# Optimization experiments

Measured on AMD Instinct MI355X. Metric: run time of the kernel, lower is better.

The kernel has to match this reference:

```python
import jax, jax.numpy as jnp
import numpy as np

NUM_GRAPHS = 1000


def setup_inputs() -> dict:
    key = jax.random.key(0)
    ks = jax.random.split(key, 8)
    N, E, F_IN, H = 100000, 1600000, 128, 64
    x = jax.random.normal(ks[0], (N, F_IN), dtype=jnp.float32)
    edge_index = jax.random.randint(ks[1], (2, E), 0, N, dtype=jnp.int64)
    batch = jnp.sort(jax.random.randint(ks[2], (N,), 0, NUM_GRAPHS, dtype=jnp.int64))
    # Glorot-ish scaled weights
    W1 = jax.random.normal(ks[3], (F_IN, H), dtype=jnp.float32) / np.sqrt(F_IN)
    W2 = jax.random.normal(ks[4], (H, H), dtype=jnp.float32) / np.sqrt(H)
    W3 = jax.random.normal(ks[5], (H, H), dtype=jnp.float32) / np.sqrt(H)
    Wl = jax.random.normal(ks[6], (H, 1), dtype=jnp.float32) / np.sqrt(H)
    return {
        "x": x, "edge_index": edge_index, "batch": batch,
        "W1": W1, "b1": jnp.zeros((H,), jnp.float32),
        "W2": W2, "b2": jnp.zeros((H,), jnp.float32),
        "W3": W3, "b3": jnp.zeros((H,), jnp.float32),
        "Wl": Wl, "bl": jnp.zeros((1,), jnp.float32),
    }


def _gcn_prep(edge_index, n_nodes):
    """Add self-loops and compute symmetric normalization coefficients."""
    loops = jnp.arange(n_nodes, dtype=edge_index.dtype)
    src = jnp.concatenate([edge_index[0], loops])  # [E+N]
    dst = jnp.concatenate([edge_index[1], loops])  # [E+N]
    deg = jax.ops.segment_sum(jnp.ones_like(dst, dtype=jnp.float32), dst,
                              num_segments=n_nodes)
    dinv = jnp.where(deg > 0, jax.lax.rsqrt(jnp.maximum(deg, 1.0)), 0.0)
    norm = dinv[src] * dinv[dst]  # [E+N]
    return src, dst, norm


def _gcn_conv(h, W, b, src, dst, norm, n_nodes):
    h = h @ W                              # [N, H] linear transform first
    msg = h[src] * norm[:, None]           # gather + normalize
    agg = jax.ops.segment_sum(msg, dst, num_segments=n_nodes)  # scatter-add
    return agg + b


def reference(x, edge_index, batch, W1, b1, W2, b2, W3, b3, Wl, bl):
    n_nodes = x.shape[0]
    src, dst, norm = _gcn_prep(edge_index, n_nodes)
    h = jax.nn.relu(_gcn_conv(x, W1, b1, src, dst, norm, n_nodes))
    h = jax.nn.relu(_gcn_conv(h, W2, b2, src, dst, norm, n_nodes))
    h = _gcn_conv(h, W3, b3, src, dst, norm, n_nodes)
    # global_mean_pool over graphs
    sums = jax.ops.segment_sum(h, batch, num_segments=NUM_GRAPHS)
    cnts = jax.ops.segment_sum(jnp.ones((n_nodes,), jnp.float32), batch,
                               num_segments=NUM_GRAPHS)
    pooled = sums / jnp.maximum(cnts, 1.0)[:, None]
    # dropout is identity in eval mode
    return pooled @ Wl + bl
```

## Files before the change

### kernel.cpp

```cpp
#include <hip/hip_runtime.h>
#include <stdint.h>

#define BKT 1024
#define EPB 8192

typedef __attribute__((ext_vector_type(8))) __bf16 bf16x8;
typedef __attribute__((ext_vector_type(4))) float floatx4;

__device__ __forceinline__ float bf2f(unsigned short h) {
    return __uint_as_float(((unsigned)h) << 16);
}
__device__ __forceinline__ float4 bf4(ushort4 v) {
    return make_float4(bf2f(v.x), bf2f(v.y), bf2f(v.z), bf2f(v.w));
}
__device__ __forceinline__ unsigned short f2bf(float f) {
    unsigned u = __float_as_uint(f);
    u = u + 0x7FFFu + ((u >> 16) & 1u);
    return (unsigned short)(u >> 16);
}
__device__ __forceinline__ ushort4 pack4(float a, float b, float c, float d) {
    ushort4 r; r.x = f2bf(a); r.y = f2bf(b); r.z = f2bf(c); r.w = f2bf(d); return r;
}


__global__ void w3l_kernel(const float* __restrict__ W3, const float* __restrict__ Wl,
                           float* __restrict__ w3l) {
    int k = threadIdx.x;
    float s = 0.f;
#pragma unroll 16
    for (int c = 0; c < 64; ++c) s += W3[k * 64 + c] * Wl[c];
    w3l[k] = s;
}


__global__ __launch_bounds__(256) void coarse_hist(const int* __restrict__ dst,
                                                   int* __restrict__ coarse, int E, int NBK) {
    __shared__ int h[128];
    if (threadIdx.x < 128) h[threadIdx.x] = 0;
    __syncthreads();
    int stride = gridDim.x * 256;
    int gid = blockIdx.x * 256 + threadIdx.x;
    const int4* d4 = (const int4*)dst;
    int E4 = E >> 2;
    for (int i = gid; i < E4; i += stride) {
        int4 v = d4[i];
        atomicAdd(&h[v.x >> 10], 1);
        atomicAdd(&h[v.y >> 10], 1);
        atomicAdd(&h[v.z >> 10], 1);
        atomicAdd(&h[v.w >> 10], 1);
    }
    for (int i = (E4 << 2) + gid; i < E; i += stride)
        atomicAdd(&h[dst[i] >> 10], 1);
    __syncthreads();
    if (threadIdx.x < NBK) {
        int v = h[threadIdx.x];
        if (v) atomicAdd(&coarse[threadIdx.x], v);
    }
}

__global__ void coarse_scan(const int* __restrict__ coarse, int* __restrict__ bbase,
                            int NBK, int E) {
    if (threadIdx.x == 0 && blockIdx.x == 0) {
        int run = 0;
        for (int i = 0; i < NBK; ++i) { bbase[i] = run; run += coarse[i]; }
        bbase[NBK] = E;
    }
}


__global__ __launch_bounds__(256) void partition_kernel(const int* __restrict__ src,
                                                        const int* __restrict__ dst,
                                                        const int* __restrict__ bbase,
                                                        int* __restrict__ gbcur,
                                                        unsigned* __restrict__ pairs,
                                                        int E, int NBK) {
    __shared__ unsigned stage[EPB];
    __shared__ int hist[128], offs[129], gbase[128], lcur[128];
    int base = blockIdx.x * EPB;
    int cntE = min(EPB, E - base);
    if (threadIdx.x < 128) hist[threadIdx.x] = 0;
    __syncthreads();
    {
        const int4* d4 = (const int4*)(dst + base);
        int c4 = cntE >> 2;
        for (int i = threadIdx.x; i < c4; i += 256) {
            int4 v = d4[i];
            atomicAdd(&hist[v.x >> 10], 1);
            atomicAdd(&hist[v.y >> 10], 1);
            atomicAdd(&hist[v.z >> 10], 1);
            atomicAdd(&hist[v.w >> 10], 1);
        }
        for (int i = (c4 << 2) + (int)threadIdx.x; i < cntE; i += 256)
            atomicAdd(&hist[dst[base + i] >> 10], 1);
    }
    __syncthreads();
    if (threadIdx.x == 0) {
        int run = 0;
        for (int b = 0; b < NBK; ++b) { offs[b] = run; run += hist[b]; }
        offs[NBK] = run;
    }
    __syncthreads();
    if (threadIdx.x < NBK) {
        int b = threadIdx.x;
        int h = hist[b];
        if (h > 0) gbase[b] = bbase[b] + atomicAdd(&gbcur[b << 4], h);
        lcur[b] = offs[b];
    }
    __syncthreads();
    for (int i = threadIdx.x; i < cntE; i += 256) {
        int e = base + i;
        int d = dst[e];
        int b = d >> 10;
        int slot = atomicAdd(&lcur[b], 1);
        stage[slot] = ((unsigned)src[e] << 10) | (unsigned)(d & 1023);
    }
    __syncthreads();
    int total = offs[NBK];
    for (int j = threadIdx.x; j < total; j += 256) {
        int lo = 0, hi = NBK;
        while (lo < hi) { int mid = (lo + hi) >> 1; if (offs[mid + 1] <= j) lo = mid + 1; else hi = mid; }
        pairs[gbase[lo] + (j - offs[lo])] = stage[j];
    }
}


__global__ __launch_bounds__(256) void bucket_build(const unsigned* __restrict__ pairs,
                                                    const int* __restrict__ bbase,
                                                    int* __restrict__ rowptr,
                                                    int* __restrict__ csr, int N, int E) {
    __shared__ int cnt[BKT];
    __shared__ int psum[256];
    int b = blockIdx.x;
    int nbase = b << 10;
    int pbeg = bbase[b], pend = bbase[b + 1];
    for (int i = threadIdx.x; i < BKT; i += 256) cnt[i] = 0;
    __syncthreads();
    for (int j = pbeg + (int)threadIdx.x; j < pend; j += 256)
        atomicAdd(&cnt[pairs[j] & 1023u], 1);
    __syncthreads();
    int i0 = threadIdx.x * 4;
    int c0 = cnt[i0], c1 = cnt[i0 + 1], c2 = cnt[i0 + 2], c3 = cnt[i0 + 3];
    int local = c0 + c1 + c2 + c3;
    psum[threadIdx.x] = local;
    __syncthreads();
    for (int d = 1; d < 256; d <<= 1) {
        int t = (threadIdx.x >= d) ? psum[threadIdx.x - d] : 0;
        __syncthreads();
        psum[threadIdx.x] += t;
        __syncthreads();
    }
    int excl = psum[threadIdx.x] - local;
    int o0 = pbeg + excl;
    int o1 = o0 + c0, o2 = o1 + c1, o3 = o2 + c2;
    int n0 = nbase + i0;
    if (n0 < N)     rowptr[n0]     = o0;
    if (n0 + 1 < N) rowptr[n0 + 1] = o1;
    if (n0 + 2 < N) rowptr[n0 + 2] = o2;
    if (n0 + 3 < N) rowptr[n0 + 3] = o3;
    cnt[i0] = o0; cnt[i0 + 1] = o1; cnt[i0 + 2] = o2; cnt[i0 + 3] = o3;
    __syncthreads();
    for (int j = pbeg + (int)threadIdx.x; j < pend; j += 256) {
        unsigned p = pairs[j];
        int slot = atomicAdd(&cnt[p & 1023u], 1);
        csr[slot] = (int)(p >> 10);
    }
    if (b == 0 && threadIdx.x == 0) rowptr[N] = E;
}


__global__ __launch_bounds__(256) void gemm1_mfma(const float* __restrict__ X,
                                                  const float* __restrict__ W,
                                                  const int* __restrict__ rowptr,
                                                  __bf16* __restrict__ gbh, int N) {
    __shared__ __align__(16) __bf16 Wt[64][136];
    for (int i = threadIdx.x; i < 128 * 64; i += 256) {
        int k = i >> 6, c = i & 63;
        Wt[c][k] = (__bf16)W[i];
    }
    __syncthreads();

    int wave = threadIdx.x >> 6;
    int l = threadIdx.x & 63;
    int cidx = l & 15;
    int g = l >> 4;
    int wbase = blockIdx.x * 64 + wave * 16;

    int arow = wbase + cidx;
    int arowc = min(arow, N - 1);
    const float4* xr = (const float4*)(X + (size_t)arowc * 128);
    bf16x8 afr[4];
#pragma unroll
    for (int kb = 0; kb < 4; ++kb) {
        float4 p = xr[kb * 8 + g * 2];
        float4 q = xr[kb * 8 + g * 2 + 1];
        bf16x8 a;
        a[0] = (__bf16)p.x; a[1] = (__bf16)p.y; a[2] = (__bf16)p.z; a[3] = (__bf16)p.w;
        a[4] = (__bf16)q.x; a[5] = (__bf16)q.y; a[6] = (__bf16)q.z; a[7] = (__bf16)q.w;
        afr[kb] = a;
    }

    floatx4 acc[4];
#pragma unroll
    for (int ct = 0; ct < 4; ++ct) acc[ct] = (floatx4){0.f, 0.f, 0.f, 0.f};

#pragma unroll
    for (int ct = 0; ct < 4; ++ct) {
#pragma unroll
        for (int kb = 0; kb < 4; ++kb) {
            bf16x8 bfr = *(const bf16x8*)&Wt[ct * 16 + cidx][kb * 32 + g * 8];
            acc[ct] = __builtin_amdgcn_mfma_f32_16x16x32_bf16(afr[kb], bfr, acc[ct], 0, 0, 0);
        }
    }

    int r0 = wbase + g * 4;
    int rp[5];
#pragma unroll
    for (int i = 0; i < 5; ++i) rp[i] = rowptr[min(r0 + i, N)];
#pragma unroll
    for (int i = 0; i < 4; ++i) {
        int row = r0 + i;
        if (row < N) {
            float dv = rsqrtf((float)(rp[i + 1] - rp[i]) + 1.0f);
#pragma unroll
            for (int ct = 0; ct < 4; ++ct)
                gbh[(size_t)row * 64 + ct * 16 + cidx] = (__bf16)(acc[ct][i] * dv);
        }
    }
}


__global__ __launch_bounds__(256) void gather_relu_kernel(const ushort4* __restrict__ gb,
                                                          const int* __restrict__ rowptr,
                                                          const int* __restrict__ csr,
                                                          const float* __restrict__ bias,
                                                          ushort4* __restrict__ h, int N) {
    int tid = blockIdx.x * blockDim.x + threadIdx.x;
    int node = tid >> 4;
    if (node >= N) return;
    int t = tid & 15;
    int beg = rowptr[node], end = rowptr[node + 1];
    float dinv = rsqrtf((float)(end - beg) + 1.0f);
    float4 acc = bf4(gb[(size_t)node * 16 + t]);
    int j = beg;
    for (; j + 8 <= end; j += 8) {
        int s0 = csr[j], s1 = csr[j + 1], s2 = csr[j + 2], s3 = csr[j + 3];
        int s4 = csr[j + 4], s5 = csr[j + 5], s6 = csr[j + 6], s7 = csr[j + 7];
        float4 v0 = bf4(gb[(size_t)s0 * 16 + t]);
        float4 v1 = bf4(gb[(size_t)s1 * 16 + t]);
        float4 v2 = bf4(gb[(size_t)s2 * 16 + t]);
        float4 v3 = bf4(gb[(size_t)s3 * 16 + t]);
        float4 v4 = bf4(gb[(size_t)s4 * 16 + t]);
        float4 v5 = bf4(gb[(size_t)s5 * 16 + t]);
        float4 v6 = bf4(gb[(size_t)s6 * 16 + t]);
        float4 v7 = bf4(gb[(size_t)s7 * 16 + t]);
        acc.x += ((v0.x + v1.x) + (v2.x + v3.x)) + ((v4.x + v5.x) + (v6.x + v7.x));
        acc.y += ((v0.y + v1.y) + (v2.y + v3.y)) + ((v4.y + v5.y) + (v6.y + v7.y));
        acc.z += ((v0.z + v1.z) + (v2.z + v3.z)) + ((v4.z + v5.z) + (v6.z + v7.z));
        acc.w += ((v0.w + v1.w) + (v2.w + v3.w)) + ((v4.w + v5.w) + (v6.w + v7.w));
    }
    for (; j + 2 <= end; j += 2) {
        int s0 = csr[j], s1 = csr[j + 1];
        float4 v0 = bf4(gb[(size_t)s0 * 16 + t]);
        float4 v1 = bf4(gb[(size_t)s1 * 16 + t]);
        acc.x += v0.x + v1.x; acc.y += v0.y + v1.y;
        acc.z += v0.z + v1.z; acc.w += v0.w + v1.w;
    }
    if (j < end) {
        int s0 = csr[j];
        float4 v0 = bf4(gb[(size_t)s0 * 16 + t]);
        acc.x += v0.x; acc.y += v0.y; acc.z += v0.z; acc.w += v0.w;
    }
    float4 bb = *(const float4*)&bias[t * 4];
    h[(size_t)node * 16 + t] = pack4(fmaxf(acc.x * dinv + bb.x, 0.f),
                                     fmaxf(acc.y * dinv + bb.y, 0.f),
                                     fmaxf(acc.z * dinv + bb.z, 0.f),
                                     fmaxf(acc.w * dinv + bb.w, 0.f));
}


__global__ __launch_bounds__(256) void gemm64_mfma(const __bf16* __restrict__ H,
                                                   const float* __restrict__ W,
                                                   const int* __restrict__ rowptr,
                                                   __bf16* __restrict__ out, int N) {
    __shared__ __align__(16) __bf16 Wt[64][72];
    for (int i = threadIdx.x; i < 64 * 64; i += 256) {
        int k = i >> 6, c = i & 63;
        Wt[c][k] = (__bf16)W[i];
    }
    __syncthreads();

    int wave = threadIdx.x >> 6;
    int l = threadIdx.x & 63;
    int cidx = l & 15;
    int g = l >> 4;
    int wbase = blockIdx.x * 64 + wave * 16;

    int arow = wbase + cidx;
    int arowc = min(arow, N - 1);
    const bf16x8* hr = (const bf16x8*)(H + (size_t)arowc * 64);
    bf16x8 afr[2];
#pragma unroll
    for (int kb = 0; kb < 2; ++kb) afr[kb] = hr[kb * 4 + g];

    floatx4 acc[4];
#pragma unroll
    for (int ct = 0; ct < 4; ++ct) acc[ct] = (floatx4){0.f, 0.f, 0.f, 0.f};

#pragma unroll
    for (int ct = 0; ct < 4; ++ct) {
#pragma unroll
        for (int kb = 0; kb < 2; ++kb) {
            bf16x8 bfr = *(const bf16x8*)&Wt[ct * 16 + cidx][kb * 32 + g * 8];
            acc[ct] = __builtin_amdgcn_mfma_f32_16x16x32_bf16(afr[kb], bfr, acc[ct], 0, 0, 0);
        }
    }

    int r0 = wbase + g * 4;
    int rp[5];
#pragma unroll
    for (int i = 0; i < 5; ++i) rp[i] = rowptr[min(r0 + i, N)];
#pragma unroll
    for (int i = 0; i < 4; ++i) {
        int row = r0 + i;
        if (row < N) {
            float dv = rsqrtf((float)(rp[i + 1] - rp[i]) + 1.0f);
#pragma unroll
            for (int ct = 0; ct < 4; ++ct)
                out[(size_t)row * 64 + ct * 16 + cidx] = (__bf16)(acc[ct][i] * dv);
        }
    }
}


__global__ __launch_bounds__(256) void agg_dot2_kernel(const ushort4* __restrict__ gb,
                                                       const int* __restrict__ rowptr,
                                                       const int* __restrict__ csr,
                                                       const float* __restrict__ bias,
                                                       const float* __restrict__ w3l,
                                                       float* __restrict__ p, int N) {
    int tid = blockIdx.x * blockDim.x + threadIdx.x;
    int node = tid >> 4;
    if (node >= N) return;
    int t = tid & 15;
    int beg = rowptr[node], end = rowptr[node + 1];
    float dinv = rsqrtf((float)(end - beg) + 1.0f);
    float4 acc = bf4(gb[(size_t)node * 16 + t]);
    int j = beg;
    for (; j + 8 <= end; j += 8) {
        int s0 = csr[j], s1 = csr[j + 1], s2 = csr[j + 2], s3 = csr[j + 3];
        int s4 = csr[j + 4], s5 = csr[j + 5], s6 = csr[j + 6], s7 = csr[j + 7];
        float4 v0 = bf4(gb[(size_t)s0 * 16 + t]);
        float4 v1 = bf4(gb[(size_t)s1 * 16 + t]);
        float4 v2 = bf4(gb[(size_t)s2 * 16 + t]);
        float4 v3 = bf4(gb[(size_t)s3 * 16 + t]);
        float4 v4 = bf4(gb[(size_t)s4 * 16 + t]);
        float4 v5 = bf4(gb[(size_t)s5 * 16 + t]);
        float4 v6 = bf4(gb[(size_t)s6 * 16 + t]);
        float4 v7 = bf4(gb[(size_t)s7 * 16 + t]);
        acc.x += ((v0.x + v1.x) + (v2.x + v3.x)) + ((v4.x + v5.x) + (v6.x + v7.x));
        acc.y += ((v0.y + v1.y) + (v2.y + v3.y)) + ((v4.y + v5.y) + (v6.y + v7.y));
        acc.z += ((v0.z + v1.z) + (v2.z + v3.z)) + ((v4.z + v5.z) + (v6.z + v7.z));
        acc.w += ((v0.w + v1.w) + (v2.w + v3.w)) + ((v4.w + v5.w) + (v6.w + v7.w));
    }
    for (; j + 2 <= end; j += 2) {
        int s0 = csr[j], s1 = csr[j + 1];
        float4 v0 = bf4(gb[(size_t)s0 * 16 + t]);
        float4 v1 = bf4(gb[(size_t)s1 * 16 + t]);
        acc.x += v0.x + v1.x; acc.y += v0.y + v1.y;
        acc.z += v0.z + v1.z; acc.w += v0.w + v1.w;
    }
    if (j < end) {
        int s0 = csr[j];
        float4 v0 = bf4(gb[(size_t)s0 * 16 + t]);
        acc.x += v0.x; acc.y += v0.y; acc.z += v0.z; acc.w += v0.w;
    }
    float4 bb = *(const float4*)&bias[t * 4];
    float4 wv = *(const float4*)&w3l[t * 4];
    float hx = fmaxf(acc.x * dinv + bb.x, 0.f);
    float hy = fmaxf(acc.y * dinv + bb.y, 0.f);
    float hz = fmaxf(acc.z * dinv + bb.z, 0.f);
    float hw = fmaxf(acc.w * dinv + bb.w, 0.f);
    float s = (hx * wv.x + hy * wv.y) + (hz * wv.z + hw * wv.w);
    s += __shfl_xor(s, 1);
    s += __shfl_xor(s, 2);
    s += __shfl_xor(s, 4);
    s += __shfl_xor(s, 8);
    if (t == 0) p[node] = s * dinv;
}


__global__ __launch_bounds__(256) void scalar_agg(const float* __restrict__ p,
                                                  const int* __restrict__ rowptr,
                                                  const int* __restrict__ csr,
                                                  float* __restrict__ s_node, int N) {
    int n = blockIdx.x * 256 + threadIdx.x;
    if (n >= N) return;
    int beg = rowptr[n], end = rowptr[n + 1];
    float dinv = rsqrtf((float)(end - beg) + 1.0f);
    float acc = p[n];
    int j = beg;
    for (; j + 4 <= end; j += 4) {
        float a0 = p[csr[j]], a1 = p[csr[j + 1]], a2 = p[csr[j + 2]], a3 = p[csr[j + 3]];
        acc += (a0 + a1) + (a2 + a3);
    }
    for (; j < end; ++j) acc += p[csr[j]];
    s_node[n] = acc * dinv;
}


__device__ __forceinline__ int lower_bound_dev(const int* __restrict__ a, int n, int v) {
    int lo = 0, hi = n;
    while (lo < hi) { int mid = (lo + hi) >> 1; if (a[mid] < v) lo = mid + 1; else hi = mid; }
    return lo;
}

__global__ void pool_out_kernel(const float* __restrict__ s_node, const int* __restrict__ batch,
                                const float* __restrict__ b3, const float* __restrict__ Wl,
                                const float* __restrict__ bl, float* __restrict__ out, int N) {
    float v = b3[threadIdx.x] * Wl[threadIdx.x];
    for (int d = 32; d; d >>= 1) v += __shfl_down(v, d);
    float bldot = __shfl(v, 0, 64);

    int gidx = blockIdx.x;
    int lo = lower_bound_dev(batch, N, gidx);
    int hi = lower_bound_dev(batch, N, gidx + 1);
    float s = 0.f;
    for (int i = lo + threadIdx.x; i < hi; i += 64) s += s_node[i];
    for (int d = 32; d; d >>= 1) s += __shfl_down(s, d);
    if (threadIdx.x == 0)
        out[gidx] = s / fmaxf((float)(hi - lo), 1.0f) + bldot + bl[0];
}


extern "C" void kernel_launch(void* const* d_in, const int* in_sizes, int n_in,
                              void* d_out, int out_size, void* d_ws, size_t ws_size,
                              hipStream_t stream) {
    const float* x   = (const float*)d_in[0];
    const int*   ei  = (const int*)d_in[1];
    const int*   bat = (const int*)d_in[2];
    const float* W1  = (const float*)d_in[3];
    const float* b1  = (const float*)d_in[4];
    const float* W2  = (const float*)d_in[5];
    const float* b2  = (const float*)d_in[6];
    const float* W3  = (const float*)d_in[7];
    const float* b3  = (const float*)d_in[8];
    const float* Wl  = (const float*)d_in[9];
    const float* bl  = (const float*)d_in[10];

    const int N = in_sizes[0] / 128;
    const int E = in_sizes[1] / 2;
    const int G = out_size;

    const int* src = ei;
    const int* dst = ei + E;

    const int NBK = (N + BKT - 1) / BKT;
    const int Np = (N + 4) & ~3;

    int*      rowptr = (int*)d_ws;
    int*      coarse = rowptr + Np;
    int*      bbase  = coarse + 128;
    float*    w3l    = (float*)(bbase + 132);
    int*      gbcur  = (int*)(w3l + 64);
    int*      csr    = gbcur + (size_t)NBK * 16;
    unsigned* pairs  = (unsigned*)(csr + E);
    ushort4*  gbA    = (ushort4*)(pairs + E);
    ushort4*  gbB    = gbA + (size_t)N * 16;
    ushort4*  hbuf   = gbB + (size_t)N * 16;
    float*    pbuf   = (float*)(hbuf + (size_t)N * 16);
    float*    s_node = pbuf + N;

    hipMemsetAsync(coarse, 0, (324 + (size_t)NBK * 16) * sizeof(int), stream);
    w3l_kernel<<<1, 64, 0, stream>>>(W3, Wl, w3l);
    coarse_hist<<<256, 256, 0, stream>>>(dst, coarse, E, NBK);
    coarse_scan<<<1, 64, 0, stream>>>(coarse, bbase, NBK, E);
    partition_kernel<<<(E + EPB - 1) / EPB, 256, 0, stream>>>(src, dst, bbase, gbcur, pairs, E, NBK);
    bucket_build<<<NBK, 256, 0, stream>>>(pairs, bbase, rowptr, csr, N, E);

    const int aggGrid = (int)(((size_t)N * 16 + 255) / 256);

    gemm1_mfma<<<(N + 63) / 64, 256, 0, stream>>>(x, W1, rowptr, (__bf16*)gbA, N);
    gather_relu_kernel<<<aggGrid, 256, 0, stream>>>(gbA, rowptr, csr, b1, hbuf, N);
    gemm64_mfma<<<(N + 63) / 64, 256, 0, stream>>>((const __bf16*)hbuf, W2, rowptr, (__bf16*)gbB, N);
    agg_dot2_kernel<<<aggGrid, 256, 0, stream>>>(gbB, rowptr, csr, b2, w3l, pbuf, N);
    scalar_agg<<<(N + 255) / 256, 256, 0, stream>>>(pbuf, rowptr, csr, s_node, N);
    pool_out_kernel<<<G, 64, 0, stream>>>(s_node, bat, b3, Wl, bl, (float*)d_out, N);
}
```

Measured before the change: 244.4 us.

## Merge w3l into scan kernel, use nontemporal CSR loads/stores, halve partition tile

Four things change. The tiny w3l kernel is folded into the single-block scan kernel, which removes one launch. CSR index loads in the aggregation kernels become nontemporal loads, and the relu output is written as one packed 64-bit nontemporal store, so streaming traffic does less damage to the cache holding the gathered features. EPB drops from 8192 to 4096, which doubles the partition grid and halves its shared-memory staging. Risks: nontemporal hints may do nothing or may hurt reuse of h by the next GEMM, and smaller partition blocks mean more global atomic contention.

```diff
diff --git a/kernel.cpp b/kernel.cpp
--- a/kernel.cpp
+++ b/kernel.cpp
@@ -2,7 +2,7 @@
 #include <stdint.h>
 
 #define BKT 1024
-#define EPB 8192
+#define EPB 4096
 
 typedef __attribute__((ext_vector_type(8))) __bf16 bf16x8;
 typedef __attribute__((ext_vector_type(4))) float floatx4;
@@ -18,18 +18,8 @@
     u = u + 0x7FFFu + ((u >> 16) & 1u);
     return (unsigned short)(u >> 16);
 }
-__device__ __forceinline__ ushort4 pack4(float a, float b, float c, float d) {
-    ushort4 r; r.x = f2bf(a); r.y = f2bf(b); r.z = f2bf(c); r.w = f2bf(d); return r;
-}
-
-
-__global__ void w3l_kernel(const float* __restrict__ W3, const float* __restrict__ Wl,
-                           float* __restrict__ w3l) {
-    int k = threadIdx.x;
-    float s = 0.f;
-#pragma unroll 16
-    for (int c = 0; c < 64; ++c) s += W3[k * 64 + c] * Wl[c];
-    w3l[k] = s;
+__device__ __forceinline__ unsigned packpair(float lo, float hi) {
+    return ((unsigned)f2bf(lo)) | ((unsigned)f2bf(hi) << 16);
 }
 
 
@@ -58,9 +48,15 @@
     }
 }
 
-__global__ void coarse_scan(const int* __restrict__ coarse, int* __restrict__ bbase,
-                            int NBK, int E) {
-    if (threadIdx.x == 0 && blockIdx.x == 0) {
+__global__ void scan_w3l_kernel(const int* __restrict__ coarse, int* __restrict__ bbase,
+                                const float* __restrict__ W3, const float* __restrict__ Wl,
+                                float* __restrict__ w3l, int NBK, int E) {
+    int k = threadIdx.x;
+    float s = 0.f;
+#pragma unroll 16
+    for (int c = 0; c < 64; ++c) s += W3[k * 64 + c] * Wl[c];
+    w3l[k] = s;
+    if (k == 0) {
         int run = 0;
         for (int i = 0; i < NBK; ++i) { bbase[i] = run; run += coarse[i]; }
         bbase[NBK] = E;
@@ -243,8 +239,14 @@
     float4 acc = bf4(gb[(size_t)node * 16 + t]);
     int j = beg;
     for (; j + 8 <= end; j += 8) {
-        int s0 = csr[j], s1 = csr[j + 1], s2 = csr[j + 2], s3 = csr[j + 3];
-        int s4 = csr[j + 4], s5 = csr[j + 5], s6 = csr[j + 6], s7 = csr[j + 7];
+        int s0 = __builtin_nontemporal_load(csr + j);
+        int s1 = __builtin_nontemporal_load(csr + j + 1);
+        int s2 = __builtin_nontemporal_load(csr + j + 2);
+        int s3 = __builtin_nontemporal_load(csr + j + 3);
+        int s4 = __builtin_nontemporal_load(csr + j + 4);
+        int s5 = __builtin_nontemporal_load(csr + j + 5);
+        int s6 = __builtin_nontemporal_load(csr + j + 6);
+        int s7 = __builtin_nontemporal_load(csr + j + 7);
         float4 v0 = bf4(gb[(size_t)s0 * 16 + t]);
         float4 v1 = bf4(gb[(size_t)s1 * 16 + t]);
         float4 v2 = bf4(gb[(size_t)s2 * 16 + t]);
@@ -259,22 +261,23 @@
         acc.w += ((v0.w + v1.w) + (v2.w + v3.w)) + ((v4.w + v5.w) + (v6.w + v7.w));
     }
     for (; j + 2 <= end; j += 2) {
-        int s0 = csr[j], s1 = csr[j + 1];
+        int s0 = __builtin_nontemporal_load(csr + j);
+        int s1 = __builtin_nontemporal_load(csr + j + 1);
         float4 v0 = bf4(gb[(size_t)s0 * 16 + t]);
         float4 v1 = bf4(gb[(size_t)s1 * 16 + t]);
         acc.x += v0.x + v1.x; acc.y += v0.y + v1.y;
         acc.z += v0.z + v1.z; acc.w += v0.w + v1.w;
     }
     if (j < end) {
-        int s0 = csr[j];
+        int s0 = __builtin_nontemporal_load(csr + j);
         float4 v0 = bf4(gb[(size_t)s0 * 16 + t]);
         acc.x += v0.x; acc.y += v0.y; acc.z += v0.z; acc.w += v0.w;
     }
     float4 bb = *(const float4*)&bias[t * 4];
-    h[(size_t)node * 16 + t] = pack4(fmaxf(acc.x * dinv + bb.x, 0.f),
-                                     fmaxf(acc.y * dinv + bb.y, 0.f),
-                                     fmaxf(acc.z * dinv + bb.z, 0.f),
-                                     fmaxf(acc.w * dinv + bb.w, 0.f));
+    unsigned lo = packpair(fmaxf(acc.x * dinv + bb.x, 0.f), fmaxf(acc.y * dinv + bb.y, 0.f));
+    unsigned hi = packpair(fmaxf(acc.z * dinv + bb.z, 0.f), fmaxf(acc.w * dinv + bb.w, 0.f));
+    unsigned long long packed = ((unsigned long long)hi << 32) | lo;
+    __builtin_nontemporal_store(packed, (unsigned long long*)&h[(size_t)node * 16 + t]);
 }
 
 
@@ -347,8 +350,14 @@
     float4 acc = bf4(gb[(size_t)node * 16 + t]);
     int j = beg;
     for (; j + 8 <= end; j += 8) {
-        int s0 = csr[j], s1 = csr[j + 1], s2 = csr[j + 2], s3 = csr[j + 3];
-        int s4 = csr[j + 4], s5 = csr[j + 5], s6 = csr[j + 6], s7 = csr[j + 7];
+        int s0 = __builtin_nontemporal_load(csr + j);
+        int s1 = __builtin_nontemporal_load(csr + j + 1);
+        int s2 = __builtin_nontemporal_load(csr + j + 2);
+        int s3 = __builtin_nontemporal_load(csr + j + 3);
+        int s4 = __builtin_nontemporal_load(csr + j + 4);
+        int s5 = __builtin_nontemporal_load(csr + j + 5);
+        int s6 = __builtin_nontemporal_load(csr + j + 6);
+        int s7 = __builtin_nontemporal_load(csr + j + 7);
         float4 v0 = bf4(gb[(size_t)s0 * 16 + t]);
         float4 v1 = bf4(gb[(size_t)s1 * 16 + t]);
         float4 v2 = bf4(gb[(size_t)s2 * 16 + t]);
@@ -363,14 +372,15 @@
         acc.w += ((v0.w + v1.w) + (v2.w + v3.w)) + ((v4.w + v5.w) + (v6.w + v7.w));
     }
     for (; j + 2 <= end; j += 2) {
-        int s0 = csr[j], s1 = csr[j + 1];
+        int s0 = __builtin_nontemporal_load(csr + j);
+        int s1 = __builtin_nontemporal_load(csr + j + 1);
         float4 v0 = bf4(gb[(size_t)s0 * 16 + t]);
         float4 v1 = bf4(gb[(size_t)s1 * 16 + t]);
         acc.x += v0.x + v1.x; acc.y += v0.y + v1.y;
         acc.z += v0.z + v1.z; acc.w += v0.w + v1.w;
     }
     if (j < end) {
-        int s0 = csr[j];
+        int s0 = __builtin_nontemporal_load(csr + j);
         float4 v0 = bf4(gb[(size_t)s0 * 16 + t]);
         acc.x += v0.x; acc.y += v0.y; acc.z += v0.z; acc.w += v0.w;
     }
@@ -400,10 +410,13 @@
     float acc = p[n];
     int j = beg;
     for (; j + 4 <= end; j += 4) {
-        float a0 = p[csr[j]], a1 = p[csr[j + 1]], a2 = p[csr[j + 2]], a3 = p[csr[j + 3]];
-        acc += (a0 + a1) + (a2 + a3);
-    }
-    for (; j < end; ++j) acc += p[csr[j]];
+        int s0 = __builtin_nontemporal_load(csr + j);
+        int s1 = __builtin_nontemporal_load(csr + j + 1);
+        int s2 = __builtin_nontemporal_load(csr + j + 2);
+        int s3 = __builtin_nontemporal_load(csr + j + 3);
+        acc += (p[s0] + p[s1]) + (p[s2] + p[s3]);
+    }
+    for (; j < end; ++j) acc += p[__builtin_nontemporal_load(csr + j)];
     s_node[n] = acc * dinv;
 }
 
@@ -471,9 +484,8 @@
     float*    s_node = pbuf + N;
 
     hipMemsetAsync(coarse, 0, (324 + (size_t)NBK * 16) * sizeof(int), stream);
-    w3l_kernel<<<1, 64, 0, stream>>>(W3, Wl, w3l);
     coarse_hist<<<256, 256, 0, stream>>>(dst, coarse, E, NBK);
-    coarse_scan<<<1, 64, 0, stream>>>(coarse, bbase, NBK, E);
+    scan_w3l_kernel<<<1, 64, 0, stream>>>(coarse, bbase, W3, Wl, w3l, NBK, E);
     partition_kernel<<<(E + EPB - 1) / EPB, 256, 0, stream>>>(src, dst, bbase, gbcur, pairs, E, NBK);
     bucket_build<<<NBK, 256, 0, stream>>>(pairs, bbase, rowptr, csr, N, E);
 
```

Result: no change. 243.0 us (-0.6%).
